# Optimization experiments

Measured on AMD Instinct MI355X. Metric: run time of the kernel, lower is better.

Reference implementation:

```python
import jax, jax.numpy as jnp
import numpy as np

B, N, E, H, DIN, DB, P, L, NB = 2, 10000, 100000, 128, 8, 16, 3, 2, 3


def setup_inputs() -> dict:
    key = jax.random.key(0)
    ks = jax.random.split(key, 16)

    def rn(i, shape, s=0.05):
        return jax.random.normal(ks[i], shape, dtype=jnp.float32) * s

    return {
        "x": jax.random.normal(ks[0], (B, DIN), dtype=jnp.float32),
        "base_features": rn(1, (N, DB), 1.0),
        "base_positions": rn(2, (N, P), 1.0),
        "Win": rn(3, (DB + DIN, H)),
        "b_in": jnp.zeros((H,), jnp.float32),
        "msg_W1": rn(4, (L, NB, 2 * H + 1, H)),
        "msg_b1": jnp.zeros((L, NB, H), jnp.float32),
        "msg_W2": rn(5, (L, NB, H, H)),
        "msg_b2": jnp.zeros((L, NB, H), jnp.float32),
        "pos_W1": rn(6, (L, NB, H, H)),
        "pos_b1": jnp.zeros((L, NB, H), jnp.float32),
        "pos_W2": rn(7, (L, NB, H, 1)),
        "pos_b2": jnp.zeros((L, NB, 1), jnp.float32),
        "upd_W1": rn(8, (L, 2 * H, H)),
        "upd_b1": jnp.zeros((L, H), jnp.float32),
        "upd_W2": rn(9, (L, H, H)),
        "upd_b2": jnp.zeros((L, H), jnp.float32),
        "out_W1": rn(10, (H, H)),
        "out_b1": jnp.zeros((H,), jnp.float32),
        "out_W2": rn(11, (H, 1)),
        "out_b2": jnp.zeros((1,), jnp.float32),
        "entity_indices": jax.random.randint(ks[12], (B,), 0, N),
        "edge_src": jax.random.randint(ks[13], (NB, E), 0, N),
        "edge_dst": jax.random.randint(ks[14], (NB, E), 0, N),
    }


def reference(x, base_features, base_positions, Win, b_in,
              msg_W1, msg_b1, msg_W2, msg_b2,
              pos_W1, pos_b1, pos_W2, pos_b2,
              upd_W1, upd_b1, upd_W2, upd_b2,
              out_W1, out_b1, out_W2, out_b2,
              entity_indices, edge_src, edge_dst):
    silu = jax.nn.silu
    b = x.shape[0]
    n = base_features.shape[0]
    # scatter each batch element's dynamic features onto its entity cell
    dynamic = jnp.zeros((b, n, x.shape[1]), x.dtype).at[jnp.arange(b), entity_indices].set(x)
    base = jnp.broadcast_to(base_features[None], (b, n, base_features.shape[1]))
    h = jnp.concatenate([base, dynamic], axis=-1) @ Win + b_in          # [B,N,H]
    p = jnp.broadcast_to(base_positions[None], (b, n, base_positions.shape[1]))  # [B,N,3]
    n_layers, n_nbhd = msg_W1.shape[0], edge_src.shape[0]
    for l in range(n_layers):
        m_sum = jnp.zeros_like(h)
        p_new = p
        for k in range(n_nbhd):
            src, dst = edge_src[k], edge_dst[k]
            # degree of aggregation target (matches torch bincount over indices[1])
            deg = jnp.clip(jnp.zeros((n,), h.dtype).at[dst].add(1.0), 1.0)[None, :, None]
            rel = p[:, dst] - p[:, src]                                  # [B,E,3]
            d2 = jnp.sum(rel * rel, axis=-1, keepdims=True)              # [B,E,1]
            m = silu(jnp.concatenate([h[:, dst], h[:, src], d2], axis=-1) @ msg_W1[l, k] + msg_b1[l, k])
            m = silu(m @ msg_W2[l, k] + msg_b2[l, k])                    # [B,E,H]
            m_sum = m_sum + jnp.zeros_like(h).at[:, dst].add(m) / deg
            coef = silu(m @ pos_W1[l, k] + pos_b1[l, k]) @ pos_W2[l, k] + pos_b2[l, k]  # [B,E,1]
            p_new = p_new + jnp.zeros_like(p).at[:, dst].add(rel * coef) / deg
        h = h + (silu(jnp.concatenate([h, m_sum], axis=-1) @ upd_W1[l] + upd_b1[l]) @ upd_W2[l] + upd_b2[l])
        p = p_new
    e = h[jnp.arange(b), entity_indices]                                 # [B,H] gather readout
    return silu(e @ out_W1 + out_b1) @ out_W2 + out_b2                   # [B,1]
```

## Files before the change

### kernel.cpp

```cpp
#include <hip/hip_runtime.h>
#include <hip/hip_bf16.h>
#include <math.h>

#define Bc   2
#define Nc   10000
#define Ec   100000
#define Hc   128
#define DINc 8
#define DBc  16
#define NBc  3
#define Lc   2
#define EB   3125

typedef float v4 __attribute__((ext_vector_type(4)));
typedef float f32x16 __attribute__((ext_vector_type(16)));
typedef _Float16 h8 __attribute__((ext_vector_type(8)));
typedef _Float16 h4 __attribute__((ext_vector_type(4)));

__device__ __forceinline__ float silu_f(float x) { return x / (1.f + __expf(-x)); }


__global__ void zero4_kernel(float* __restrict__ p, int n4) {
  int i = blockIdx.x * blockDim.x + threadIdx.x;
  if (i < n4) ((v4*)p)[i] = (v4)(0.f);
}

__global__ void copy_kernel(float* __restrict__ dst, const float* __restrict__ src, int n) {
  int i = blockIdx.x * blockDim.x + threadIdx.x;
  if (i < n) dst[i] = src[i];
}


__global__ void hist_kernel(int* __restrict__ hist, const int* __restrict__ edst) {
  int i = blockIdx.x * blockDim.x + threadIdx.x;
  if (i < NBc * Ec) {
    int k = i / Ec;
    atomicAdd(&hist[k * Nc + edst[i]], 1);
  }
}

__global__ void scan_kernel(const int* __restrict__ hist, int* __restrict__ offs,
                            float* __restrict__ deginv) {
  const int k = blockIdx.x, tid = threadIdx.x;
  const int NPT = 40;
  __shared__ int part[256];
  int local[NPT];
  int sum = 0;
  for (int j = 0; j < NPT; ++j) {
    int n = tid * NPT + j;
    if (n < Nc) { local[j] = sum; sum += hist[k * Nc + n]; }
  }
  part[tid] = sum;
  __syncthreads();
  for (int off = 1; off < 256; off <<= 1) {
    int v = (tid >= off) ? part[tid - off] : 0;
    __syncthreads();
    part[tid] += v;
    __syncthreads();
  }
  int excl = part[tid] - sum;
  for (int j = 0; j < NPT; ++j) {
    int n = tid * NPT + j;
    if (n < Nc) {
      offs[k * Nc + n] = excl + local[j];
      deginv[k * Nc + n] = 1.f / fmaxf((float)hist[k * Nc + n], 1.f);
    }
  }
}

__global__ void sort_scatter_kernel(int* __restrict__ sorted, int* __restrict__ cursor,
                                    const int* __restrict__ offs, const int* __restrict__ edst) {
  int i = blockIdx.x * blockDim.x + threadIdx.x;
  if (i < NBc * Ec) {
    int k = i / Ec, e = i - k * Ec;
    int d = edst[i];
    int pos = offs[k * Nc + d] + atomicAdd(&cursor[k * Nc + d], 1);
    sorted[k * Ec + pos] = e;
  }
}


__global__ void init_h_kernel(_Float16* __restrict__ h16, const float* __restrict__ bfeat,
                              const float* __restrict__ x, const float* __restrict__ Win,
                              const float* __restrict__ b_in, const int* __restrict__ ent) {
  int g = blockIdx.x * blockDim.x + threadIdx.x;
  if (g >= Bc * Nc * Hc) return;
  int j = g & (Hc - 1);
  int bn = g >> 7;
  int n = bn % Nc;
  int b = bn / Nc;
  float acc = b_in[j];
#pragma unroll
  for (int i = 0; i < DBc; ++i) acc = fmaf(bfeat[n * DBc + i], Win[i * Hc + j], acc);
  if (n == ent[b]) {
#pragma unroll
    for (int i = 0; i < DINc; ++i) acc = fmaf(x[b * DINc + i], Win[(DBc + i) * Hc + j], acc);
  }
  h16[g] = (_Float16)acc;
}

__global__ void init_p_kernel(float* __restrict__ p, const float* __restrict__ bp) {
  int i = blockIdx.x * blockDim.x + threadIdx.x;
  if (i < Bc * Nc * 3) p[i] = bp[i % (Nc * 3)];
}

__global__ void conv_frag_kernel(_Float16* __restrict__ dst, const float* __restrict__ src,
                                 int nchunk, int total, long srcStride) {
  int g = blockIdx.x * blockDim.x + threadIdx.x;
  if (g >= total) return;
  int j = g & 7;
  int lane = (g >> 3) & 63;
  int q = g >> 9;
  int t = q % nchunk;
  int q2 = q / nchunk;
  int wave = q2 & 3;
  int mat = q2 >> 2;
  int kk = t * 16 + (lane >> 5) * 8 + j;
  int col = wave * 32 + (lane & 31);
  dst[g] = (_Float16)src[(size_t)mat * srcStride + (size_t)kk * Hc + col];
}


__global__ __launch_bounds__(256, 8)
void edge_mfma_kernel(const _Float16* __restrict__ h16, const float* __restrict__ p,
                      float* __restrict__ m_sum, float* __restrict__ p_new,
                      const float* __restrict__ deginv,
                      const int* __restrict__ esrc, const int* __restrict__ edst,
                      const int* __restrict__ sorted,
                      const _Float16* __restrict__ W1f, const _Float16* __restrict__ W2f,
                      const _Float16* __restrict__ P1f,
                      const float* __restrict__ mW1, const float* __restrict__ mb1,
                      const float* __restrict__ mb2, const float* __restrict__ pb1,
                      const float* __restrict__ pW2, const float* __restrict__ pb2,
                      int l) {
  const int k = blockIdx.y, lk = l * NBc + k;
  const int b = (blockIdx.x >= EB) ? 1 : 0;
  const int pos0 = (blockIdx.x - b * EB) << 5;
  const int tid = threadIdx.x;
  const int wave = tid >> 6, lane = tid & 63;
  const int lrow = lane & 31, lhalf = lane >> 5;

  __shared__ __align__(16) _Float16 Abuf[32 * 256];
  __shared__ int shd[32], shs[32], sdi[32];
  __shared__ float sd2[32], sdinvs[32], srel[32][3], scoef[32];
  __shared__ float cw1[Hc], cb1[Hc], cb2[Hc], cpb1[Hc], cpw2[Hc];

  if (tid < Hc) {
    cw1[tid]  = mW1[((size_t)lk * 257 + 256) * Hc + tid];
    cb1[tid]  = mb1[lk * Hc + tid];
    cb2[tid]  = mb2[lk * Hc + tid];
    cpb1[tid] = pb1[lk * Hc + tid];
    cpw2[tid] = pW2[lk * Hc + tid];
  }
  if (tid < 32) {
    int e = sorted[k * Ec + pos0 + tid];
    int si = esrc[k * Ec + e], di = edst[k * Ec + e];
    int nd = b * Nc + di, ns = b * Nc + si;
    const float* pd = &p[(size_t)nd * 3];
    const float* ps = &p[(size_t)ns * 3];
    float rx = pd[0] - ps[0], ry = pd[1] - ps[1], rz = pd[2] - ps[2];
    srel[tid][0] = rx; srel[tid][1] = ry; srel[tid][2] = rz;
    sd2[tid] = rx * rx + ry * ry + rz * rz;
    sdinvs[tid] = deginv[k * Nc + di];
    sdi[tid] = di;
    shd[tid] = nd * Hc; shs[tid] = ns * Hc;
    scoef[tid] = 0.f;
  }
  __syncthreads();

  {
    const int i = tid >> 3, c = tid & 7;
    const int sw = (i & 7) << 4;
    char* ab = (char*)Abuf;
    h8 v0 = *(const h8*)&h16[shd[i] + c * 8];
    h8 v1 = *(const h8*)&h16[shd[i] + 64 + c * 8];
    h8 v2 = *(const h8*)&h16[shs[i] + c * 8];
    h8 v3 = *(const h8*)&h16[shs[i] + 64 + c * 8];
    *(h8*)(ab + (i << 9) + ((c * 16) ^ sw)) = v0;
    *(h8*)(ab + (i << 9) + 128 + ((c * 16) ^ sw)) = v1;
    *(h8*)(ab + (i << 9) + 256 + ((c * 16) ^ sw)) = v2;
    *(h8*)(ab + (i << 9) + 384 + ((c * 16) ^ sw)) = v3;
  }
  __syncthreads();

  const int swz = (lrow & 7) << 4;
  const char* abc = (const char*)Abuf;
  char* abw = (char*)Abuf;

  f32x16 acc;
#pragma unroll
  for (int r = 0; r < 16; ++r) acc[r] = 0.f;
#pragma unroll
  for (int t = 0; t < 16; ++t) {
    int off = (t << 5) + (lhalf << 4);
    h8 bact = *(const h8*)(abc + (lrow << 9) + ((off & 0x180)) + ((off & 0x70) ^ swz));
    h8 aw = *(const h8*)&W1f[((((size_t)lk * 4 + wave) * 16 + t) << 9) + (lane << 3)];
    acc = __builtin_amdgcn_mfma_f32_32x32x16_f16(aw, bact, acc, 0, 0, 0);
  }
  h4 m1pk[4];
  {
    float d2e = sd2[lrow];
#pragma unroll
    for (int c = 0; c < 4; ++c) {
      int hb = (wave << 5) + (c << 3) + (lhalf << 2);
#pragma unroll
      for (int z = 0; z < 4; ++z)
        m1pk[c][z] = (_Float16)silu_f(acc[c * 4 + z] + d2e * cw1[hb + z] + cb1[hb + z]);
    }
  }
  __syncthreads();
  {
#pragma unroll
    for (int c = 0; c < 4; ++c) {
      int hb = (wave << 5) + (c << 3) + (lhalf << 2);
      *(h4*)(abw + (lrow << 9) + 256 + (((hb << 1)) ^ swz)) = m1pk[c];
    }
  }
  __syncthreads();

  f32x16 acc2;
#pragma unroll
  for (int r = 0; r < 16; ++r) acc2[r] = 0.f;
#pragma unroll
  for (int t = 0; t < 8; ++t) {
    h8 bact = *(const h8*)(abc + (lrow << 9) + 256 + ((((t << 5) + (lhalf << 4))) ^ swz));
    h8 aw = *(const h8*)&W2f[((((size_t)lk * 4 + wave) * 8 + t) << 9) + (lane << 3)];
    acc2 = __builtin_amdgcn_mfma_f32_32x32x16_f16(aw, bact, acc2, 0, 0, 0);
  }
  {
#pragma unroll
    for (int c = 0; c < 4; ++c) {
      int hb = (wave << 5) + (c << 3) + (lhalf << 2);
      h4 pk;
#pragma unroll
      for (int z = 0; z < 4; ++z)
        pk[z] = (_Float16)silu_f(acc2[c * 4 + z] + cb2[hb + z]);
      *(h4*)(abw + (lrow << 9) + (((hb << 1)) ^ swz)) = pk;
    }
  }
  __syncthreads();

  f32x16 acc3;
#pragma unroll
  for (int r = 0; r < 16; ++r) acc3[r] = 0.f;
#pragma unroll
  for (int t = 0; t < 8; ++t) {
    h8 bact = *(const h8*)(abc + (lrow << 9) + ((((t << 5) + (lhalf << 4))) ^ swz));
    h8 aw = *(const h8*)&P1f[((((size_t)lk * 4 + wave) * 8 + t) << 9) + (lane << 3)];
    acc3 = __builtin_amdgcn_mfma_f32_32x32x16_f16(aw, bact, acc3, 0, 0, 0);
  }
  {
    float csum = 0.f;
#pragma unroll
    for (int r = 0; r < 16; ++r) {
      int hg = (wave << 5) + (r & 3) + (((r >> 2)) << 3) + (lhalf << 2);
      csum += silu_f(acc3[r] + cpb1[hg]) * cpw2[hg];
    }
    csum += __shfl_down(csum, 32);
    if (lane < 32) atomicAdd(&scoef[lrow], csum);
  }
  __syncthreads();

  {
    const int col = tid & 127;
    const int r0 = (tid >> 7) << 4;
    const size_t bbase = (size_t)b * Nc * Hc;
    float accv = 0.f, cinv = 0.f;
    int cur = -1;
    for (int r = r0; r < r0 + 16; ++r) {
      float v = (float)*(const _Float16*)(abc + (r << 9) + (((col << 1)) ^ ((r & 7) << 4)));
      int d = sdi[r];
      if (d != cur) {
        if (cur >= 0) atomicAdd(&m_sum[bbase + (size_t)cur * Hc + col], accv * cinv);
        cur = d; cinv = sdinvs[r]; accv = v;
      } else accv += v;
    }
    atomicAdd(&m_sum[bbase + (size_t)cur * Hc + col], accv * cinv);
  }
  if (tid < 32) {
    float cf = (scoef[tid] + pb2[lk]) * sdinvs[tid];
    float* pp = &p_new[((size_t)(b * Nc + sdi[tid])) * 3];
    atomicAdd(&pp[0], srel[tid][0] * cf);
    atomicAdd(&pp[1], srel[tid][1] * cf);
    atomicAdd(&pp[2], srel[tid][2] * cf);
  }
}


__global__ __launch_bounds__(256, 8)
void update_mfma_kernel(_Float16* __restrict__ h16, const float* __restrict__ m_sum,
                        const _Float16* __restrict__ U1f, const _Float16* __restrict__ U2f,
                        const float* __restrict__ ub1, const float* __restrict__ ub2, int l) {
  const int tid = threadIdx.x;
  const int wave = tid >> 6, lane = tid & 63;
  const int lrow = lane & 31, lhalf = lane >> 5;
  const int row0 = blockIdx.x << 5;

  __shared__ __align__(16) _Float16 Abuf[32 * 256];
  __shared__ float cu1[Hc], cu2[Hc];

  if (tid < Hc) { cu1[tid] = ub1[l * Hc + tid]; cu2[tid] = ub2[l * Hc + tid]; }

  {
    const int i = tid >> 3, c = tid & 7;
    const int sw = (i & 7) << 4;
    char* ab = (char*)Abuf;
    size_t hb = (size_t)(row0 + i) * Hc;
    h8 v0 = *(const h8*)&h16[hb + c * 8];
    h8 v1 = *(const h8*)&h16[hb + 64 + c * 8];
    *(h8*)(ab + (i << 9) + ((c * 16) ^ sw)) = v0;
    *(h8*)(ab + (i << 9) + 128 + ((c * 16) ^ sw)) = v1;
#pragma unroll
    for (int q = 0; q < 4; ++q) {
      v4 mv = *(const v4*)&m_sum[hb + c * 4 + q * 32];
      h4 mh;
#pragma unroll
      for (int z = 0; z < 4; ++z) mh[z] = (_Float16)mv[z];
      *(h4*)(ab + (i << 9) + 256 + ((q * 64 + c * 8) ^ sw)) = mh;
    }
  }
  __syncthreads();

  const int swz = (lrow & 7) << 4;
  const char* abc = (const char*)Abuf;
  char* abw = (char*)Abuf;

  f32x16 acc;
#pragma unroll
  for (int r = 0; r < 16; ++r) acc[r] = 0.f;
#pragma unroll
  for (int t = 0; t < 16; ++t) {
    int off = (t << 5) + (lhalf << 4);
    h8 bact = *(const h8*)(abc + (lrow << 9) + ((off & 0x180)) + ((off & 0x70) ^ swz));
    h8 aw = *(const h8*)&U1f[((((size_t)l * 4 + wave) * 16 + t) << 9) + (lane << 3)];
    acc = __builtin_amdgcn_mfma_f32_32x32x16_f16(aw, bact, acc, 0, 0, 0);
  }
  h4 u1pk[4];
  {
#pragma unroll
    for (int c = 0; c < 4; ++c) {
      int hb = (wave << 5) + (c << 3) + (lhalf << 2);
#pragma unroll
      for (int z = 0; z < 4; ++z)
        u1pk[c][z] = (_Float16)silu_f(acc[c * 4 + z] + cu1[hb + z]);
    }
  }
  __syncthreads();
  {
#pragma unroll
    for (int c = 0; c < 4; ++c) {
      int hb = (wave << 5) + (c << 3) + (lhalf << 2);
      *(h4*)(abw + (lrow << 9) + 256 + (((hb << 1)) ^ swz)) = u1pk[c];
    }
  }
  __syncthreads();

  f32x16 acc2;
#pragma unroll
  for (int r = 0; r < 16; ++r) acc2[r] = 0.f;
#pragma unroll
  for (int t = 0; t < 8; ++t) {
    h8 bact = *(const h8*)(abc + (lrow << 9) + 256 + ((((t << 5) + (lhalf << 4))) ^ swz));
    h8 aw = *(const h8*)&U2f[((((size_t)l * 4 + wave) * 8 + t) << 9) + (lane << 3)];
    acc2 = __builtin_amdgcn_mfma_f32_32x32x16_f16(aw, bact, acc2, 0, 0, 0);
  }
  {
    _Float16* hp = &h16[(size_t)(row0 + lrow) * Hc];
#pragma unroll
    for (int c = 0; c < 4; ++c) {
      int hb = (wave << 5) + (c << 3) + (lhalf << 2);
      h4 old = *(const h4*)&hp[hb];
      h4 nv;
#pragma unroll
      for (int z = 0; z < 4; ++z)
        nv[z] = (_Float16)((float)old[z] + acc2[c * 4 + z] + cu2[hb + z]);
      *(h4*)&hp[hb] = nv;
    }
  }
}


__global__ void readout_kernel(const _Float16* __restrict__ h16, const int* __restrict__ ent,
                               const float* __restrict__ oW1, const float* __restrict__ ob1,
                               const float* __restrict__ oW2, const float* __restrict__ ob2,
                               float* __restrict__ out) {
  __shared__ float tb[Bc][Hc];
  int tid = threadIdx.x;
  int b = tid >> 7, j = tid & 127;
  const _Float16* e = &h16[((size_t)(b * Nc + ent[b])) * Hc];
  float a = ob1[j];
#pragma unroll 4
  for (int i = 0; i < Hc; ++i) a = fmaf((float)e[i], oW1[i * Hc + j], a);
  tb[b][j] = silu_f(a);
  __syncthreads();
  if (tid < Bc) {
    float s = ob2[0];
    for (int i = 0; i < Hc; ++i) s = fmaf(tb[tid][i], oW2[i], s);
    out[tid] = s;
  }
}


extern "C" void kernel_launch(void* const* d_in, const int* in_sizes, int n_in,
                              void* d_out, int out_size, void* d_ws, size_t ws_size,
                              hipStream_t stream) {
  const float* x    = (const float*)d_in[0];
  const float* bfe  = (const float*)d_in[1];
  const float* bp   = (const float*)d_in[2];
  const float* Win  = (const float*)d_in[3];
  const float* b_in = (const float*)d_in[4];
  const float* mW1  = (const float*)d_in[5];
  const float* mb1  = (const float*)d_in[6];
  const float* mW2  = (const float*)d_in[7];
  const float* mb2  = (const float*)d_in[8];
  const float* pW1  = (const float*)d_in[9];
  const float* pb1  = (const float*)d_in[10];
  const float* pW2  = (const float*)d_in[11];
  const float* pb2  = (const float*)d_in[12];
  const float* uW1  = (const float*)d_in[13];
  const float* ub1  = (const float*)d_in[14];
  const float* uW2  = (const float*)d_in[15];
  const float* ub2  = (const float*)d_in[16];
  const float* oW1  = (const float*)d_in[17];
  const float* ob1  = (const float*)d_in[18];
  const float* oW2  = (const float*)d_in[19];
  const float* ob2  = (const float*)d_in[20];
  const int* ent    = (const int*)d_in[21];
  const int* esrc   = (const int*)d_in[22];
  const int* edst   = (const int*)d_in[23];

  float* wsf = (float*)d_ws;
  float* msum   = wsf;  wsf += (size_t)Bc * Nc * Hc;
  float* pa     = wsf;  wsf += (size_t)Bc * Nc * 3;
  float* pb_    = wsf;  wsf += (size_t)Bc * Nc * 3;
  float* deginv = wsf;  wsf += (size_t)NBc * Nc;
  _Float16* h16 = (_Float16*)wsf;
  _Float16* W1f = h16 + (size_t)Bc * Nc * Hc;
  _Float16* W2f = W1f + 196608;
  _Float16* P1f = W2f + 98304;
  _Float16* U1f = P1f + 98304;
  _Float16* U2f = U1f + 65536;
  int* hist   = (int*)(U2f + 32768);
  int* cursor = hist + NBc * Nc;
  int* offs   = cursor + NBc * Nc;
  int* sorted = offs + NBc * Nc;

  zero4_kernel<<<dim3((2 * NBc * Nc / 4 + 255) / 256), dim3(256), 0, stream>>>((float*)hist, 2 * NBc * Nc / 4);
  hist_kernel<<<dim3((NBc * Ec + 255) / 256), dim3(256), 0, stream>>>(hist, edst);
  scan_kernel<<<dim3(NBc), dim3(256), 0, stream>>>(hist, offs, deginv);
  sort_scatter_kernel<<<dim3((NBc * Ec + 255) / 256), dim3(256), 0, stream>>>(sorted, cursor, offs, edst);

  conv_frag_kernel<<<dim3(768), dim3(256), 0, stream>>>(W1f, mW1, 16, 196608, 257L * 128);
  conv_frag_kernel<<<dim3(384), dim3(256), 0, stream>>>(W2f, mW2, 8, 98304, 128L * 128);
  conv_frag_kernel<<<dim3(384), dim3(256), 0, stream>>>(P1f, pW1, 8, 98304, 128L * 128);
  conv_frag_kernel<<<dim3(256), dim3(256), 0, stream>>>(U1f, uW1, 16, 65536, 256L * 128);
  conv_frag_kernel<<<dim3(128), dim3(256), 0, stream>>>(U2f, uW2, 8, 32768, 128L * 128);

  init_h_kernel<<<dim3((Bc * Nc * Hc + 255) / 256), dim3(256), 0, stream>>>(h16, bfe, x, Win, b_in, ent);
  init_p_kernel<<<dim3((Bc * Nc * 3 + 255) / 256), dim3(256), 0, stream>>>(pa, bp);

  float* pcur = pa;
  float* pnew = pb_;
  const int nmh = Bc * Nc * Hc;
  for (int l = 0; l < Lc; ++l) {
    zero4_kernel<<<dim3((nmh / 4 + 255) / 256), dim3(256), 0, stream>>>(msum, nmh / 4);
    copy_kernel<<<dim3((Bc * Nc * 3 + 255) / 256), dim3(256), 0, stream>>>(pnew, pcur, Bc * Nc * 3);
    edge_mfma_kernel<<<dim3(Bc * EB, NBc), dim3(256), 0, stream>>>(
        h16, pcur, msum, pnew, deginv, esrc, edst, sorted,
        W1f, W2f, P1f, mW1, mb1, mb2, pb1, pW2, pb2, l);
    update_mfma_kernel<<<dim3(Bc * Nc / 32), dim3(256), 0, stream>>>(h16, msum, U1f, U2f, ub1, ub2, l);
    float* t = pcur; pcur = pnew; pnew = t;
  }
  readout_kernel<<<dim3(1), dim3(256), 0, stream>>>(h16, ent, oW1, ob1, oW2, ob2, (float*)d_out);
}
```

Before: 695.7 us.

## Fold biases and d2 term into extra MFMA K-chunk, relayout LDS fragments

Each weight matrix is extended with an extra 16-row K chunk that holds the d2 weight row and the bias row. A small constant activation chunk (d2, 1, zeros) then lets the MFMA add bias and distance terms, so the per-element scalar bias adds and their shared-memory staging go away. LDS activations are stored directly in MFMA fragment order to make reads contiguous. The segmented scatter uses a precomputed ballot flush mask, and silu uses rcp with packed conversions. The extra MFMA per GEMM adds some work, and rounding bias and d2 to fp16 with rtz conversion changes numerics slightly.

```diff
diff --git a/kernel.cpp b/kernel.cpp
--- a/kernel.cpp
+++ b/kernel.cpp
@@ -17,7 +17,17 @@
 typedef _Float16 h8 __attribute__((ext_vector_type(8)));
 typedef _Float16 h4 __attribute__((ext_vector_type(4)));
 
-__device__ __forceinline__ float silu_f(float x) { return x / (1.f + __expf(-x)); }
+__device__ __forceinline__ float silu_f(float x) {
+  return x * __builtin_amdgcn_rcpf(1.f + __expf(-x));
+}
+
+__device__ __forceinline__ h4 pack4(float a, float b, float c, float d) {
+  typedef decltype(__builtin_amdgcn_cvt_pkrtz(0.f, 0.f)) pk2;
+  union { h4 v; pk2 p[2]; } u;
+  u.p[0] = __builtin_amdgcn_cvt_pkrtz(a, b);
+  u.p[1] = __builtin_amdgcn_cvt_pkrtz(c, d);
+  return u.v;
+}
 
 
 __global__ void zero4_kernel(float* __restrict__ p, int n4) {
@@ -104,8 +114,9 @@
   if (i < Bc * Nc * 3) p[i] = bp[i % (Nc * 3)];
 }
 
-__global__ void conv_frag_kernel(_Float16* __restrict__ dst, const float* __restrict__ src,
-                                 int nchunk, int total, long srcStride) {
+__global__ void conv_ext_kernel(_Float16* __restrict__ dst, const float* __restrict__ src,
+                                const float* __restrict__ bias,
+                                int nchunk, int total, int realRows, int biasRow) {
   int g = blockIdx.x * blockDim.x + threadIdx.x;
   if (g >= total) return;
   int j = g & 7;
@@ -116,8 +127,11 @@
   int wave = q2 & 3;
   int mat = q2 >> 2;
   int kk = t * 16 + (lane >> 5) * 8 + j;
-  int col = wave * 32 + (lane & 31);
-  dst[g] = (_Float16)src[(size_t)mat * srcStride + (size_t)kk * Hc + col];
+  int col = (wave << 5) + (lane & 31);
+  float v = 0.f;
+  if (kk < realRows)      v = src[((size_t)mat * realRows + kk) * Hc + col];
+  else if (kk == biasRow) v = bias[mat * Hc + col];
+  dst[g] = (_Float16)v;
 }
 
 
@@ -127,10 +141,8 @@
                       const float* __restrict__ deginv,
                       const int* __restrict__ esrc, const int* __restrict__ edst,
                       const int* __restrict__ sorted,
-                      const _Float16* __restrict__ W1f, const _Float16* __restrict__ W2f,
-                      const _Float16* __restrict__ P1f,
-                      const float* __restrict__ mW1, const float* __restrict__ mb1,
-                      const float* __restrict__ mb2, const float* __restrict__ pb1,
+                      const _Float16* __restrict__ W1e, const _Float16* __restrict__ W2e,
+                      const _Float16* __restrict__ P1e,
                       const float* __restrict__ pW2, const float* __restrict__ pb2,
                       int l) {
   const int k = blockIdx.y, lk = l * NBc + k;
@@ -140,18 +152,14 @@
   const int wave = tid >> 6, lane = tid & 63;
   const int lrow = lane & 31, lhalf = lane >> 5;
 
-  __shared__ __align__(16) _Float16 Abuf[32 * 256];
+  __shared__ __align__(16) _Float16 RegA[16 * 512];
+  __shared__ __align__(16) _Float16 Dchk[512];
   __shared__ int shd[32], shs[32], sdi[32];
-  __shared__ float sd2[32], sdinvs[32], srel[32][3], scoef[32];
-  __shared__ float cw1[Hc], cb1[Hc], cb2[Hc], cpb1[Hc], cpw2[Hc];
-
-  if (tid < Hc) {
-    cw1[tid]  = mW1[((size_t)lk * 257 + 256) * Hc + tid];
-    cb1[tid]  = mb1[lk * Hc + tid];
-    cb2[tid]  = mb2[lk * Hc + tid];
-    cpb1[tid] = pb1[lk * Hc + tid];
-    cpw2[tid] = pW2[lk * Hc + tid];
-  }
+  __shared__ float sdinvs[32], srel[32][3], scoef[32];
+  __shared__ float cpw2[Hc];
+  __shared__ unsigned sflush;
+
+  if (tid < Hc) cpw2[tid] = pW2[lk * Hc + tid];
   if (tid < 32) {
     int e = sorted[k * Ec + pos0 + tid];
     int si = esrc[k * Ec + e], di = edst[k * Ec + e];
@@ -160,101 +168,123 @@
     const float* ps = &p[(size_t)ns * 3];
     float rx = pd[0] - ps[0], ry = pd[1] - ps[1], rz = pd[2] - ps[2];
     srel[tid][0] = rx; srel[tid][1] = ry; srel[tid][2] = rz;
-    sd2[tid] = rx * rx + ry * ry + rz * rz;
+    float d2 = rx * rx + ry * ry + rz * rz;
     sdinvs[tid] = deginv[k * Nc + di];
     sdi[tid] = di;
     shd[tid] = nd * Hc; shs[tid] = ns * Hc;
     scoef[tid] = 0.f;
-  }
-  __syncthreads();
-
-  {
-    const int i = tid >> 3, c = tid & 7;
-    const int sw = (i & 7) << 4;
-    char* ab = (char*)Abuf;
+    h8 dv = (h8)(_Float16)0.f;
+    dv[0] = (_Float16)d2; dv[1] = (_Float16)1.f;
+    *(h8*)&Dchk[tid * 8] = dv;
+    int prev = __shfl_up(di, 1);
+    bool isStart = (tid == 0) || (di != prev);
+    unsigned long long m = __ballot(isStart);
+    if (tid == 0) sflush = (unsigned)((m >> 1) | 0x80000000ull);
+  } else if (tid < 64) {
+    h8 dv = (h8)(_Float16)0.f;
+    *(h8*)&Dchk[tid * 8] = dv;
+  }
+  __syncthreads();
+
+  {
+    const int i = tid & 31, c = tid >> 5;
     h8 v0 = *(const h8*)&h16[shd[i] + c * 8];
     h8 v1 = *(const h8*)&h16[shd[i] + 64 + c * 8];
     h8 v2 = *(const h8*)&h16[shs[i] + c * 8];
     h8 v3 = *(const h8*)&h16[shs[i] + 64 + c * 8];
-    *(h8*)(ab + (i << 9) + ((c * 16) ^ sw)) = v0;
-    *(h8*)(ab + (i << 9) + 128 + ((c * 16) ^ sw)) = v1;
-    *(h8*)(ab + (i << 9) + 256 + ((c * 16) ^ sw)) = v2;
-    *(h8*)(ab + (i << 9) + 384 + ((c * 16) ^ sw)) = v3;
-  }
-  __syncthreads();
-
-  const int swz = (lrow & 7) << 4;
-  const char* abc = (const char*)Abuf;
-  char* abw = (char*)Abuf;
-
+    int slot = (i + ((c & 1) << 5)) << 3;
+    int tb = (c >> 1) << 9;
+    *(h8*)&RegA[tb + 0 * 2048 + slot] = v0;
+    *(h8*)&RegA[tb + 4 * 512  + slot] = v1;
+    *(h8*)&RegA[tb + 8 * 512  + slot] = v2;
+    *(h8*)&RegA[tb + 12 * 512 + slot] = v3;
+  }
+  __syncthreads();
+
+  const _Float16* wb1 = &W1e[(size_t)(lk * 4 + wave) * (17 * 512)];
   f32x16 acc;
 #pragma unroll
   for (int r = 0; r < 16; ++r) acc[r] = 0.f;
 #pragma unroll
   for (int t = 0; t < 16; ++t) {
-    int off = (t << 5) + (lhalf << 4);
-    h8 bact = *(const h8*)(abc + (lrow << 9) + ((off & 0x180)) + ((off & 0x70) ^ swz));
-    h8 aw = *(const h8*)&W1f[((((size_t)lk * 4 + wave) * 16 + t) << 9) + (lane << 3)];
+    h8 bact = *(const h8*)&RegA[t * 512 + lane * 8];
+    h8 aw   = *(const h8*)&wb1[t * 512 + lane * 8];
     acc = __builtin_amdgcn_mfma_f32_32x32x16_f16(aw, bact, acc, 0, 0, 0);
   }
+  {
+    h8 bact = *(const h8*)&Dchk[lane * 8];
+    h8 aw   = *(const h8*)&wb1[16 * 512 + lane * 8];
+    acc = __builtin_amdgcn_mfma_f32_32x32x16_f16(aw, bact, acc, 0, 0, 0);
+  }
   h4 m1pk[4];
-  {
-    float d2e = sd2[lrow];
+#pragma unroll
+  for (int c = 0; c < 4; ++c)
+    m1pk[c] = pack4(silu_f(acc[c * 4 + 0]), silu_f(acc[c * 4 + 1]),
+                    silu_f(acc[c * 4 + 2]), silu_f(acc[c * 4 + 3]));
+  __syncthreads();
+#pragma unroll
+  for (int c = 0; c < 4; ++c) {
+    int t = (wave << 1) + (c >> 1);
+    int slot = lrow + ((c & 1) << 5);
+    *(h4*)&RegA[t * 512 + slot * 8 + lhalf * 4] = m1pk[c];
+  }
+  __syncthreads();
+
+  const _Float16* wb2 = &W2e[(size_t)(lk * 4 + wave) * (9 * 512)];
+  f32x16 acc2;
+#pragma unroll
+  for (int r = 0; r < 16; ++r) acc2[r] = 0.f;
+#pragma unroll
+  for (int t = 0; t < 8; ++t) {
+    h8 bact = *(const h8*)&RegA[t * 512 + lane * 8];
+    h8 aw   = *(const h8*)&wb2[t * 512 + lane * 8];
+    acc2 = __builtin_amdgcn_mfma_f32_32x32x16_f16(aw, bact, acc2, 0, 0, 0);
+  }
+  {
+    h8 bact = *(const h8*)&Dchk[lane * 8];
+    h8 aw   = *(const h8*)&wb2[8 * 512 + lane * 8];
+    acc2 = __builtin_amdgcn_mfma_f32_32x32x16_f16(aw, bact, acc2, 0, 0, 0);
+  }
+  h4 m2pk[4];
+#pragma unroll
+  for (int c = 0; c < 4; ++c) {
+    m2pk[c] = pack4(silu_f(acc2[c * 4 + 0]), silu_f(acc2[c * 4 + 1]),
+                    silu_f(acc2[c * 4 + 2]), silu_f(acc2[c * 4 + 3]));
+    int t = 8 + (wave << 1) + (c >> 1);
+    int slot = lrow + ((c & 1) << 5);
+    *(h4*)&RegA[t * 512 + slot * 8 + lhalf * 4] = m2pk[c];
+  }
+  __syncthreads();
+  {
+    char* rm = (char*)RegA;
 #pragma unroll
     for (int c = 0; c < 4; ++c) {
       int hb = (wave << 5) + (c << 3) + (lhalf << 2);
-#pragma unroll
-      for (int z = 0; z < 4; ++z)
-        m1pk[c][z] = (_Float16)silu_f(acc[c * 4 + z] + d2e * cw1[hb + z] + cb1[hb + z]);
+      *(h4*)(rm + (lrow << 8) + (((hb << 1)) ^ ((lrow & 15) << 4))) = m2pk[c];
     }
   }
-  __syncthreads();
-  {
-#pragma unroll
-    for (int c = 0; c < 4; ++c) {
-      int hb = (wave << 5) + (c << 3) + (lhalf << 2);
-      *(h4*)(abw + (lrow << 9) + 256 + (((hb << 1)) ^ swz)) = m1pk[c];
-    }
-  }
-  __syncthreads();
-
-  f32x16 acc2;
-#pragma unroll
-  for (int r = 0; r < 16; ++r) acc2[r] = 0.f;
+
+  const _Float16* wb3 = &P1e[(size_t)(lk * 4 + wave) * (9 * 512)];
+  f32x16 acc3;
+#pragma unroll
+  for (int r = 0; r < 16; ++r) acc3[r] = 0.f;
 #pragma unroll
   for (int t = 0; t < 8; ++t) {
-    h8 bact = *(const h8*)(abc + (lrow << 9) + 256 + ((((t << 5) + (lhalf << 4))) ^ swz));
-    h8 aw = *(const h8*)&W2f[((((size_t)lk * 4 + wave) * 8 + t) << 9) + (lane << 3)];
-    acc2 = __builtin_amdgcn_mfma_f32_32x32x16_f16(aw, bact, acc2, 0, 0, 0);
-  }
-  {
-#pragma unroll
-    for (int c = 0; c < 4; ++c) {
-      int hb = (wave << 5) + (c << 3) + (lhalf << 2);
-      h4 pk;
-#pragma unroll
-      for (int z = 0; z < 4; ++z)
-        pk[z] = (_Float16)silu_f(acc2[c * 4 + z] + cb2[hb + z]);
-      *(h4*)(abw + (lrow << 9) + (((hb << 1)) ^ swz)) = pk;
-    }
-  }
-  __syncthreads();
-
-  f32x16 acc3;
-#pragma unroll
-  for (int r = 0; r < 16; ++r) acc3[r] = 0.f;
-#pragma unroll
-  for (int t = 0; t < 8; ++t) {
-    h8 bact = *(const h8*)(abc + (lrow << 9) + ((((t << 5) + (lhalf << 4))) ^ swz));
-    h8 aw = *(const h8*)&P1f[((((size_t)lk * 4 + wave) * 8 + t) << 9) + (lane << 3)];
+    h8 bact = *(const h8*)&RegA[(8 + t) * 512 + lane * 8];
+    h8 aw   = *(const h8*)&wb3[t * 512 + lane * 8];
     acc3 = __builtin_amdgcn_mfma_f32_32x32x16_f16(aw, bact, acc3, 0, 0, 0);
   }
   {
+    h8 bact = *(const h8*)&Dchk[lane * 8];
+    h8 aw   = *(const h8*)&wb3[8 * 512 + lane * 8];
+    acc3 = __builtin_amdgcn_mfma_f32_32x32x16_f16(aw, bact, acc3, 0, 0, 0);
+  }
+  {
     float csum = 0.f;
 #pragma unroll
     for (int r = 0; r < 16; ++r) {
-      int hg = (wave << 5) + (r & 3) + (((r >> 2)) << 3) + (lhalf << 2);
-      csum += silu_f(acc3[r] + cpb1[hg]) * cpw2[hg];
+      int hg = (wave << 5) + (r & 3) + ((r >> 2) << 3) + (lhalf << 2);
+      csum += silu_f(acc3[r]) * cpw2[hg];
     }
     csum += __shfl_down(csum, 32);
     if (lane < 32) atomicAdd(&scoef[lrow], csum);
@@ -265,17 +295,21 @@
     const int col = tid & 127;
     const int r0 = (tid >> 7) << 4;
     const size_t bbase = (size_t)b * Nc * Hc;
-    float accv = 0.f, cinv = 0.f;
-    int cur = -1;
-    for (int r = r0; r < r0 + 16; ++r) {
-      float v = (float)*(const _Float16*)(abc + (r << 9) + (((col << 1)) ^ ((r & 7) << 4)));
-      int d = sdi[r];
-      if (d != cur) {
-        if (cur >= 0) atomicAdd(&m_sum[bbase + (size_t)cur * Hc + col], accv * cinv);
-        cur = d; cinv = sdinvs[r]; accv = v;
-      } else accv += v;
+    const unsigned fm = sflush;
+    const char* rm = (const char*)RegA;
+    float accv = 0.f;
+#pragma unroll
+    for (int rr = 0; rr < 16; ++rr) {
+      int r = r0 + rr;
+      float v = (float)*(const _Float16*)(rm + (r << 8) + (((col << 1)) ^ ((r & 15) << 4)));
+      accv += v;
+      if ((fm >> r) & 1u) {
+        atomicAdd(&m_sum[bbase + (size_t)sdi[r] * Hc + col], accv * sdinvs[r]);
+        accv = 0.f;
+      }
     }
-    atomicAdd(&m_sum[bbase + (size_t)cur * Hc + col], accv * cinv);
+    if (r0 == 0 && !((fm >> 15) & 1u))
+      atomicAdd(&m_sum[bbase + (size_t)sdi[15] * Hc + col], accv * sdinvs[15]);
   }
   if (tid < 32) {
     float cf = (scoef[tid] + pb2[lk]) * sdinvs[tid];
@@ -289,79 +323,86 @@
 
 __global__ __launch_bounds__(256, 8)
 void update_mfma_kernel(_Float16* __restrict__ h16, const float* __restrict__ m_sum,
-                        const _Float16* __restrict__ U1f, const _Float16* __restrict__ U2f,
-                        const float* __restrict__ ub1, const float* __restrict__ ub2, int l) {
+                        const _Float16* __restrict__ U1e, const _Float16* __restrict__ U2e,
+                        int l) {
   const int tid = threadIdx.x;
   const int wave = tid >> 6, lane = tid & 63;
   const int lrow = lane & 31, lhalf = lane >> 5;
   const int row0 = blockIdx.x << 5;
 
-  __shared__ __align__(16) _Float16 Abuf[32 * 256];
-  __shared__ float cu1[Hc], cu2[Hc];
-
-  if (tid < Hc) { cu1[tid] = ub1[l * Hc + tid]; cu2[tid] = ub2[l * Hc + tid]; }
-
-  {
-    const int i = tid >> 3, c = tid & 7;
-    const int sw = (i & 7) << 4;
-    char* ab = (char*)Abuf;
+  __shared__ __align__(16) _Float16 RegA[16 * 512];
+  __shared__ __align__(16) _Float16 Dchk[512];
+
+  if (tid < 64) {
+    h8 dv = (h8)(_Float16)0.f;
+    if (tid < 32) dv[1] = (_Float16)1.f;
+    *(h8*)&Dchk[tid * 8] = dv;
+  }
+  {
+    const int i = tid & 31, c = tid >> 5;
     size_t hb = (size_t)(row0 + i) * Hc;
     h8 v0 = *(const h8*)&h16[hb + c * 8];
     h8 v1 = *(const h8*)&h16[hb + 64 + c * 8];
-    *(h8*)(ab + (i << 9) + ((c * 16) ^ sw)) = v0;
-    *(h8*)(ab + (i << 9) + 128 + ((c * 16) ^ sw)) = v1;
-#pragma unroll
-    for (int q = 0; q < 4; ++q) {
-      v4 mv = *(const v4*)&m_sum[hb + c * 4 + q * 32];
-      h4 mh;
-#pragma unroll
-      for (int z = 0; z < 4; ++z) mh[z] = (_Float16)mv[z];
-      *(h4*)(ab + (i << 9) + 256 + ((q * 64 + c * 8) ^ sw)) = mh;
-    }
-  }
-  __syncthreads();
-
-  const int swz = (lrow & 7) << 4;
-  const char* abc = (const char*)Abuf;
-  char* abw = (char*)Abuf;
-
+    v4 m0 = *(const v4*)&m_sum[hb + c * 8];
+    v4 m1 = *(const v4*)&m_sum[hb + c * 8 + 4];
+    v4 m2 = *(const v4*)&m_sum[hb + 64 + c * 8];
+    v4 m3 = *(const v4*)&m_sum[hb + 64 + c * 8 + 4];
+    union { h8 v; h4 q[2]; } w0, w1;
+    w0.q[0] = pack4(m0[0], m0[1], m0[2], m0[3]);
+    w0.q[1] = pack4(m1[0], m1[1], m1[2], m1[3]);
+    w1.q[0] = pack4(m2[0], m2[1], m2[2], m2[3]);
+    w1.q[1] = pack4(m3[0], m3[1], m3[2], m3[3]);
+    int slot = (i + ((c & 1) << 5)) << 3;
+    int tb = (c >> 1) << 9;
+    *(h8*)&RegA[tb + slot] = v0;
+    *(h8*)&RegA[tb + 4 * 512 + slot] = v1;
+    *(h8*)&RegA[tb + 8 * 512 + slot] = w0.v;
+    *(h8*)&RegA[tb + 12 * 512 + slot] = w1.v;
+  }
+  __syncthreads();
+
+  const _Float16* wb1 = &U1e[(size_t)(l * 4 + wave) * (17 * 512)];
   f32x16 acc;
 #pragma unroll
   for (int r = 0; r < 16; ++r) acc[r] = 0.f;
 #pragma unroll
   for (int t = 0; t < 16; ++t) {
-    int off = (t << 5) + (lhalf << 4);
-    h8 bact = *(const h8*)(abc + (lrow << 9) + ((off & 0x180)) + ((off & 0x70) ^ swz));
-    h8 aw = *(const h8*)&U1f[((((size_t)l * 4 + wave) * 16 + t) << 9) + (lane << 3)];
+    h8 bact = *(const h8*)&RegA[t * 512 + lane * 8];
+    h8 aw   = *(const h8*)&wb1[t * 512 + lane * 8];
     acc = __builtin_amdgcn_mfma_f32_32x32x16_f16(aw, bact, acc, 0, 0, 0);
   }
+  {
+    h8 bact = *(const h8*)&Dchk[lane * 8];
+    h8 aw   = *(const h8*)&wb1[16 * 512 + lane * 8];
+    acc = __builtin_amdgcn_mfma_f32_32x32x16_f16(aw, bact, acc, 0, 0, 0);
+  }
   h4 u1pk[4];
-  {
-#pragma unroll
-    for (int c = 0; c < 4; ++c) {
-      int hb = (wave << 5) + (c << 3) + (lhalf << 2);
-#pragma unroll
-      for (int z = 0; z < 4; ++z)
-        u1pk[c][z] = (_Float16)silu_f(acc[c * 4 + z] + cu1[hb + z]);
-    }
-  }
-  __syncthreads();
-  {
-#pragma unroll
-    for (int c = 0; c < 4; ++c) {
-      int hb = (wave << 5) + (c << 3) + (lhalf << 2);
-      *(h4*)(abw + (lrow << 9) + 256 + (((hb << 1)) ^ swz)) = u1pk[c];
-    }
-  }
-  __syncthreads();
-
+#pragma unroll
+  for (int c = 0; c < 4; ++c)
+    u1pk[c] = pack4(silu_f(acc[c * 4 + 0]), silu_f(acc[c * 4 + 1]),
+                    silu_f(acc[c * 4 + 2]), silu_f(acc[c * 4 + 3]));
+  __syncthreads();
+#pragma unroll
+  for (int c = 0; c < 4; ++c) {
+    int t = (wave << 1) + (c >> 1);
+    int slot = lrow + ((c & 1) << 5);
+    *(h4*)&RegA[t * 512 + slot * 8 + lhalf * 4] = u1pk[c];
+  }
+  __syncthreads();
+
+  const _Float16* wb2 = &U2e[(size_t)(l * 4 + wave) * (9 * 512)];
   f32x16 acc2;
 #pragma unroll
   for (int r = 0; r < 16; ++r) acc2[r] = 0.f;
 #pragma unroll
   for (int t = 0; t < 8; ++t) {
-    h8 bact = *(const h8*)(abc + (lrow << 9) + 256 + ((((t << 5) + (lhalf << 4))) ^ swz));
-    h8 aw = *(const h8*)&U2f[((((size_t)l * 4 + wave) * 8 + t) << 9) + (lane << 3)];
+    h8 bact = *(const h8*)&RegA[t * 512 + lane * 8];
+    h8 aw   = *(const h8*)&wb2[t * 512 + lane * 8];
+    acc2 = __builtin_amdgcn_mfma_f32_32x32x16_f16(aw, bact, acc2, 0, 0, 0);
+  }
+  {
+    h8 bact = *(const h8*)&Dchk[lane * 8];
+    h8 aw   = *(const h8*)&wb2[8 * 512 + lane * 8];
     acc2 = __builtin_amdgcn_mfma_f32_32x32x16_f16(aw, bact, acc2, 0, 0, 0);
   }
   {
@@ -370,11 +411,8 @@
     for (int c = 0; c < 4; ++c) {
       int hb = (wave << 5) + (c << 3) + (lhalf << 2);
       h4 old = *(const h4*)&hp[hb];
-      h4 nv;
-#pragma unroll
-      for (int z = 0; z < 4; ++z)
-        nv[z] = (_Float16)((float)old[z] + acc2[c * 4 + z] + cu2[hb + z]);
-      *(h4*)&hp[hb] = nv;
+      *(h4*)&hp[hb] = pack4((float)old[0] + acc2[c * 4 + 0], (float)old[1] + acc2[c * 4 + 1],
+                            (float)old[2] + acc2[c * 4 + 2], (float)old[3] + acc2[c * 4 + 3]);
     }
   }
 }
@@ -435,12 +473,12 @@
   float* pb_    = wsf;  wsf += (size_t)Bc * Nc * 3;
   float* deginv = wsf;  wsf += (size_t)NBc * Nc;
   _Float16* h16 = (_Float16*)wsf;
-  _Float16* W1f = h16 + (size_t)Bc * Nc * Hc;
-  _Float16* W2f = W1f + 196608;
-  _Float16* P1f = W2f + 98304;
-  _Float16* U1f = P1f + 98304;
-  _Float16* U2f = U1f + 65536;
-  int* hist   = (int*)(U2f + 32768);
+  _Float16* W1e = h16 + (size_t)Bc * Nc * Hc;
+  _Float16* W2e = W1e + 208896;
+  _Float16* P1e = W2e + 110592;
+  _Float16* U1e = P1e + 110592;
+  _Float16* U2e = U1e + 69632;
+  int* hist   = (int*)(U2e + 36864);
   int* cursor = hist + NBc * Nc;
   int* offs   = cursor + NBc * Nc;
   int* sorted = offs + NBc * Nc;
@@ -450,11 +488,11 @@
   scan_kernel<<<dim3(NBc), dim3(256), 0, stream>>>(hist, offs, deginv);
   sort_scatter_kernel<<<dim3((NBc * Ec + 255) / 256), dim3(256), 0, stream>>>(sorted, cursor, offs, edst);
 
-  conv_frag_kernel<<<dim3(768), dim3(256), 0, stream>>>(W1f, mW1, 16, 196608, 257L * 128);
-  conv_frag_kernel<<<dim3(384), dim3(256), 0, stream>>>(W2f, mW2, 8, 98304, 128L * 128);
-  conv_frag_kernel<<<dim3(384), dim3(256), 0, stream>>>(P1f, pW1, 8, 98304, 128L * 128);
-  conv_frag_kernel<<<dim3(256), dim3(256), 0, stream>>>(U1f, uW1, 16, 65536, 256L * 128);
-  conv_frag_kernel<<<dim3(128), dim3(256), 0, stream>>>(U2f, uW2, 8, 32768, 128L * 128);
+  conv_ext_kernel<<<dim3(816), dim3(256), 0, stream>>>(W1e, mW1, mb1, 17, 208896, 257, 257);
+  conv_ext_kernel<<<dim3(432), dim3(256), 0, stream>>>(W2e, mW2, mb2, 9, 110592, 128, 129);
+  conv_ext_kernel<<<dim3(432), dim3(256), 0, stream>>>(P1e, pW1, pb1, 9, 110592, 128, 129);
+  conv_ext_kernel<<<dim3(272), dim3(256), 0, stream>>>(U1e, uW1, ub1, 17, 69632, 256, 257);
+  conv_ext_kernel<<<dim3(144), dim3(256), 0, stream>>>(U2e, uW2, ub2, 9, 36864, 128, 129);
 
   init_h_kernel<<<dim3((Bc * Nc * Hc + 255) / 256), dim3(256), 0, stream>>>(h16, bfe, x, Win, b_in, ent);
   init_p_kernel<<<dim3((Bc * Nc * 3 + 255) / 256), dim3(256), 0, stream>>>(pa, bp);
@@ -467,8 +505,8 @@
     copy_kernel<<<dim3((Bc * Nc * 3 + 255) / 256), dim3(256), 0, stream>>>(pnew, pcur, Bc * Nc * 3);
     edge_mfma_kernel<<<dim3(Bc * EB, NBc), dim3(256), 0, stream>>>(
         h16, pcur, msum, pnew, deginv, esrc, edst, sorted,
-        W1f, W2f, P1f, mW1, mb1, mb2, pb1, pW2, pb2, l);
-    update_mfma_kernel<<<dim3(Bc * Nc / 32), dim3(256), 0, stream>>>(h16, msum, U1f, U2f, ub1, ub2, l);
+        W1e, W2e, P1e, pW2, pb2, l);
+    update_mfma_kernel<<<dim3(Bc * Nc / 32), dim3(256), 0, stream>>>(h16, msum, U1e, U2e, l);
     float* t = pcur; pcur = pnew; pnew = t;
   }
   readout_kernel<<<dim3(1), dim3(256), 0, stream>>>(h16, ent, oW1, ob1, oW2, ob2, (float*)d_out);
```

Result: faster. 672.1 us (-3.4%).
